# Optimization experiments

Hardware: AMD Instinct MI355X
Metric: run time of the kernel (lower is better)

## Reference

```python
import jax, jax.numpy as jnp
import numpy as np

TAU_PAIR = 1.5
TAU_ATTN = 1.5
TAU_SS = 1.25
TOPK = 3
WIN = 8
EPS = 1e-8
NEG = -10000.0


def _linear(x, w, b):
    return x @ w.T + b


def _mlp2(x, w1, b1, w2, b2):
    return _linear(jax.nn.gelu(_linear(x, w1, b1), approximate=False), w2, b2)


def _layernorm(x, g, b, eps=1e-5):
    m = jnp.mean(x, axis=-1, keepdims=True)
    v = jnp.var(x, axis=-1, keepdims=True)
    return (x - m) / jnp.sqrt(v + eps) * g + b


def _win_mean(vals, mask, radius):
    # vals, mask: (B, L); masked windowed mean via conv1d with ones kernel
    K = 2 * radius + 1
    kern = jnp.ones((1, 1, K), vals.dtype)
    conv = lambda a: jax.lax.conv_general_dilated(
        a, kern, (1,), [(radius, radius)], dimension_numbers=('NCH', 'OIH', 'NCH'))
    sx = conv((vals * mask)[:, None, :])
    sm = conv(mask[:, None, :])
    return (sx / jnp.maximum(sm, 1.0))[:, 0]


def setup_inputs() -> dict:
    key = jax.random.key(0)
    ks = jax.random.split(key, 32)
    B, L, D = 4, 2048, 512
    R = 32
    PLU = R * (R - 1) // 2        # 496
    CURV = 16
    CH1 = max(CURV * 2, PLU // 2)  # 248
    CONT_IN = 3 * D + CURV        # 1552
    CONTENT, STATS_D, BOT = 64, 32, 64
    STATS_IN = 10 + 3 + 8         # N_STATS_V2 + ss_prob + ss_logit_proj

    def w(k, shape):
        return jax.random.normal(k, shape, jnp.float32) * 0.05

    return {
        'H_geom': jax.random.normal(ks[0], (B, L, D), jnp.float32),
        'pair_logits': jax.random.normal(ks[1], (B, L, L), jnp.float32),
        'ss_logits': jax.random.normal(ks[2], (B, L, 3), jnp.float32),
        'kappa_last': jax.random.normal(ks[3], (B, L, PLU), jnp.float32),
        'seq_mask': jnp.ones((B, L), dtype=bool),
        'curv_w1': w(ks[4], (CH1, PLU)), 'curv_b1': jnp.zeros((CH1,), jnp.float32),
        'curv_w2': w(ks[5], (CURV, CH1)), 'curv_b2': jnp.zeros((CURV,), jnp.float32),
        'sslp_w': w(ks[6], (8, 3)), 'sslp_b': jnp.zeros((8,), jnp.float32),
        'ln_g': jnp.ones((10,), jnp.float32), 'ln_b': jnp.zeros((10,), jnp.float32),
        'cont_w1': w(ks[7], (CONTENT * 2, CONT_IN)), 'cont_b1': jnp.zeros((CONTENT * 2,), jnp.float32),
        'cont_w2': w(ks[8], (CONTENT, CONTENT * 2)), 'cont_b2': jnp.zeros((CONTENT,), jnp.float32),
        'stats_w1': w(ks[9], (STATS_D * 2, STATS_IN)), 'stats_b1': jnp.zeros((STATS_D * 2,), jnp.float32),
        'stats_w2': w(ks[10], (STATS_D, STATS_D * 2)), 'stats_b2': jnp.zeros((STATS_D,), jnp.float32),
        'merge_w1': w(ks[11], (BOT * 2, CONTENT + STATS_D)), 'merge_b1': jnp.zeros((BOT * 2,), jnp.float32),
        'merge_w2': w(ks[12], (BOT, BOT * 2)), 'merge_b2': jnp.zeros((BOT,), jnp.float32),
    }


def _forward(H_geom, pair_logits, ss_logits, kappa_last, seq_mask,
             curv_w1, curv_b1, curv_w2, curv_b2, sslp_w, sslp_b, ln_g, ln_b,
             cont_w1, cont_b1, cont_w2, cont_b2, stats_w1, stats_b1, stats_w2, stats_b2,
             merge_w1, merge_b1, merge_w2, merge_b2):
    mf = seq_mask.astype(jnp.float32)  # (B, L)
    B, L, D = H_geom.shape
    smb = seq_mask.astype(bool)
    diag = jnp.eye(L, dtype=bool)[None]
    invalid = diag | (~smb)[:, None, :] | (~smb)[:, :, None]  # (B, L, L)
    clean = jnp.where(invalid, NEG, pair_logits)

    curv = _mlp2(kappa_last, curv_w1, curv_b1, curv_w2, curv_b2)  # (B, L, 16)

    pair_prob = jax.nn.sigmoid(clean / TAU_PAIR)
    pair_attn = jnp.nan_to_num(jax.nn.softmax(clean / TAU_ATTN, axis=-1), nan=0.0)
    pair_entropy = -(pair_attn * jnp.log(pair_attn + EPS)).sum(-1, keepdims=True)
    max_pair_prob = pair_prob.max(-1, keepdims=True)
    unpaired = 1.0 - max_pair_prob
    valid_pair = (~invalid).astype(jnp.float32)
    n_valid = jnp.maximum(valid_pair.sum(-1, keepdims=True), 1.0)
    pair_mass = pair_prob.sum(-1, keepdims=True) / n_valid

    ss_prob = jax.nn.softmax(ss_logits / TAU_SS, axis=-1)
    ss_entropy = -(ss_prob * jnp.log(ss_prob + EPS)).sum(-1, keepdims=True)
    log_n = jnp.maximum(jnp.log(n_valid), 1e-4)
    pen = jnp.nan_to_num(jnp.clip(pair_entropy / log_n, 0.0, 1.0), nan=0.0)
    ss_lp = _linear(ss_logits, sslp_w, sslp_b)

    ctx_mean = jnp.einsum('bij,bjd->bid', pair_attn, H_geom)

    k = min(TOPK, L)
    tv, ti = jax.lax.top_k(clean, k)  # (B, L, k)
    tvalid = (tv > -9000.0).astype(jnp.float32)
    tw = jax.nn.softmax(jnp.where(tvalid == 0, NEG, tv) / TAU_ATTN, axis=-1) * tvalid
    tw = tw / jnp.maximum(tw.sum(-1, keepdims=True), EPS)
    tw = jnp.nan_to_num(tw, nan=0.0)
    H_topk = jax.vmap(lambda h, i: h[i])(H_geom, ti)  # (B, L, k, D)
    ctx_topk = (tw[..., None] * H_topk).sum(axis=2)

    idx = jnp.arange(L)
    dist = jnp.abs(idx[:, None] - idx[None, :]).astype(jnp.float32)[None]
    local = (dist <= WIN).astype(jnp.float32)
    distal = (dist > WIN).astype(jnp.float32)
    n_local = jnp.maximum((valid_pair * local).sum(-1, keepdims=True), 1.0)
    n_distal = jnp.maximum((valid_pair * distal).sum(-1, keepdims=True), 1.0)
    local_mass = (pair_prob * local).sum(-1, keepdims=True) / n_local
    distal_mass = (pair_prob * distal).sum(-1, keepdims=True) / n_distal

    win_up3 = _win_mean(unpaired[..., 0], mf, 2)[..., None]
    win_up7 = _win_mean(unpaired[..., 0], mf, 5)[..., None]
    win_ent7 = _win_mean(pen[..., 0], mf, 5)[..., None]

    stats = jnp.concatenate([
        pair_mass, max_pair_prob, unpaired, pen, ss_entropy,
        local_mass, distal_mass, win_up3, win_up7, win_ent7], axis=-1) * mf[..., None]
    stats = jnp.nan_to_num(stats, nan=0.0, posinf=1.0, neginf=0.0)

    content_in = jnp.concatenate([H_geom, ctx_mean, ctx_topk, curv], axis=-1)
    stats_in = jnp.concatenate([_layernorm(stats, ln_g, ln_b), ss_prob, ss_lp], axis=-1)
    ch = _mlp2(content_in, cont_w1, cont_b1, cont_w2, cont_b2)
    sh = _mlp2(stats_in, stats_w1, stats_b1, stats_w2, stats_b2)
    B_tok = _mlp2(jnp.concatenate([ch, sh], axis=-1), merge_w1, merge_b1, merge_w2, merge_b2)
    B_tok = B_tok * mf[..., None]
    return B_tok, stats


def reference(H_geom, pair_logits, ss_logits, kappa_last, seq_mask,
              curv_w1, curv_b1, curv_w2, curv_b2, sslp_w, sslp_b, ln_g, ln_b,
              cont_w1, cont_b1, cont_w2, cont_b2, stats_w1, stats_b1, stats_w2, stats_b2,
              merge_w1, merge_b1, merge_w2, merge_b2):
    return _forward(H_geom, pair_logits, ss_logits, kappa_last, seq_mask,
                    curv_w1, curv_b1, curv_w2, curv_b2, sslp_w, sslp_b, ln_g, ln_b,
                    cont_w1, cont_b1, cont_w2, cont_b2, stats_w1, stats_b1, stats_w2, stats_b2,
                    merge_w1, merge_b1, merge_w2, merge_b2)
```

## Files before the change

kernel.cpp:

```cpp
#include <hip/hip_runtime.h>
#include <hip/hip_bf16.h>

#define BN 4
#define LL 2048
#define DD 512
#define BLROWS 8192
#define CI_LD 1792

typedef __attribute__((ext_vector_type(8))) short s8v;
typedef __attribute__((ext_vector_type(4))) short s4v;
typedef __attribute__((ext_vector_type(4))) float f4v;

#define GF_GELU    1
#define GF_OUTBF16 2
#define GF_SCALE   4
#define GF_BIAS    8

static __device__ __forceinline__ float frcp(float x) { return __builtin_amdgcn_rcpf(x); }

template<int C>
static __device__ __forceinline__ float fdpp0(float x) {
    return __builtin_bit_cast(float, __builtin_amdgcn_update_dpp(
        0, __builtin_bit_cast(int, x), C, 0xf, 0xf, false));
}
static __device__ __forceinline__ float wave_sum(float x) {
    x += fdpp0<0x111>(x);
    x += fdpp0<0x112>(x);
    x += fdpp0<0x114>(x);
    x += fdpp0<0x118>(x);
    x += fdpp0<0x142>(x);
    x += fdpp0<0x143>(x);
    return __builtin_bit_cast(float, __builtin_amdgcn_readlane(__builtin_bit_cast(int, x), 63));
}
template<int C>
static __device__ __forceinline__ void amax_lev(unsigned& bk, int& bj) {
    unsigned ok = (unsigned)__builtin_amdgcn_update_dpp(0, (int)bk, C, 0xf, 0xf, false);
    int      oj = __builtin_amdgcn_update_dpp(0x7fffffff, bj, C, 0xf, 0xf, false);
    bool take = (ok > bk) || (ok == bk && oj < bj);
    bk = take ? ok : bk;
    bj = take ? oj : bj;
}

struct Seg2 {
    const float* src;
    __hip_bfloat16* dst;
    int srows, scols, sld, drows, dld, pcols, doff, blk0;
};
struct ConvArgs2 {
    Seg2 s[9];
    int nseg;
};

__global__ __launch_bounds__(256) void mega1(
    ConvArgs2 a, int nconv,
    const float* __restrict__ pair, const float* __restrict__ H,
    __hip_bfloat16* __restrict__ E, __hip_bfloat16* __restrict__ ci,
    float* __restrict__ invZ, float* __restrict__ pen, float* __restrict__ unp,
    float* __restrict__ sigs, float* __restrict__ sigloc, float* __restrict__ mpp,
    __hip_bfloat16* __restrict__ Ht,
    const float* __restrict__ curv_w2, const float* __restrict__ cont_w1,
    const float* __restrict__ curv_b2, const float* __restrict__ cont_b1,
    __hip_bfloat16* __restrict__ cont_w1b, float* __restrict__ cbias2)
{
    __shared__ float tile[64][36];
    int bid = blockIdx.x;

    if (bid < 2048) {
        int wid = threadIdx.x >> 6, lane = threadIdx.x & 63;
        int g = bid * 4 + wid;
        int i = g & (LL - 1);
        const float* row = pair + (size_t)g * LL;
        int lb = lane << 2;

        float tt[32];
        float ssig = 0.f, sloc = 0.f, T = 0.f, U = 0.f;
        #pragma unroll
        for (int k = 0; k < 8; ++k) {
            float4 v = *(const float4*)(row + k * 256 + lb);
            float cv4[4] = {v.x, v.y, v.z, v.w};
            #pragma unroll
            for (int t = 0; t < 4; ++t) {
                int j = k * 256 + lb + t;
                float cv = cv4[t];
                float e = __expf(cv * 0.66666667f);
                e = (j == i) ? 0.0f : e;
                tt[k * 4 + t] = e;
                T += e;
                U = fmaf(e, cv, U);
                float sg = e * frcp(1.0f + e);
                ssig += sg;
                int dd = j - i;
                sloc += ((unsigned)(dd + 8) <= 16u) ? sg : 0.0f;
            }
        }
        T    = wave_sum(T);
        U    = wave_sum(U);
        ssig = wave_sum(ssig);
        sloc = wave_sum(sloc);

        int f0 = -1, f1 = -1;
        int fidx[3]; float fval[3];
        #pragma unroll
        for (int p = 0; p < 3; ++p) {
            unsigned bk = 0u; int bj = 0x7fffffff;
            #pragma unroll
            for (int k = 0; k < 8; ++k) {
                #pragma unroll
                for (int t = 0; t < 4; ++t) {
                    int j = k * 256 + lb + t;
                    unsigned mk = __float_as_uint(tt[k * 4 + t]);
                    mk = (j != f0 && j != f1) ? mk : 0u;
                    bool take = (mk > bk) || (mk == bk && j < bj);
                    bk = take ? mk : bk;
                    bj = take ? j : bj;
                }
            }
            amax_lev<0x111>(bk, bj);
            amax_lev<0x112>(bk, bj);
            amax_lev<0x114>(bk, bj);
            amax_lev<0x118>(bk, bj);
            amax_lev<0x142>(bk, bj);
            amax_lev<0x143>(bk, bj);
            unsigned kk = (unsigned)__builtin_amdgcn_readlane((int)bk, 63);
            int jj = __builtin_amdgcn_readlane(bj, 63);
            fval[p] = __uint_as_float(kk);
            fidx[p] = jj;
            if (p == 0) f0 = jj;
            if (p == 1) f1 = jj;
        }
        float t0v = fval[0];
        float s = frcp(t0v);

        short* Eg = (short*)E + (size_t)g * LL;
        #pragma unroll
        for (int k = 0; k < 8; ++k) {
            s4v ev;
            #pragma unroll
            for (int t = 0; t < 4; ++t) {
                __hip_bfloat16 hb = __float2bfloat16(tt[k * 4 + t] * s);
                ev[t] = *(short*)&hb;
            }
            *(s4v*)(Eg + k * 256 + lb) = ev;
        }

        float e1 = fval[1] * s;
        float e2 = fval[2] * s;
        float inv = frcp(1.0f + e1 + e2);
        float w0 = inv, w1 = e1 * inv, w2 = e2 * inv;
        int b = g >> 11;
        const float* Hb = H + (size_t)b * LL * DD;
        int dcol = lane << 3;
        const float* r0p = Hb + (size_t)fidx[0] * DD + dcol;
        const float* r1p = Hb + (size_t)fidx[1] * DD + dcol;
        const float* r2p = Hb + (size_t)fidx[2] * DD + dcol;
        float4 a0 = *(const float4*)(r0p), a1 = *(const float4*)(r0p + 4);
        float4 b0 = *(const float4*)(r1p), b1 = *(const float4*)(r1p + 4);
        float4 c0 = *(const float4*)(r2p), c1 = *(const float4*)(r2p + 4);
        s8v ov;
        float o8[8] = {w0*a0.x + w1*b0.x + w2*c0.x, w0*a0.y + w1*b0.y + w2*c0.y,
                       w0*a0.z + w1*b0.z + w2*c0.z, w0*a0.w + w1*b0.w + w2*c0.w,
                       w0*a1.x + w1*b1.x + w2*c1.x, w0*a1.y + w1*b1.y + w2*c1.y,
                       w0*a1.z + w1*b1.z + w2*c1.z, w0*a1.w + w1*b1.w + w2*c1.w};
        #pragma unroll
        for (int t = 0; t < 8; ++t) {
            __hip_bfloat16 hb = __float2bfloat16(o8[t]);
            ov[t] = *(short*)&hb;
        }
        *(s8v*)((short*)ci + (size_t)g * CI_LD + 1024 + dcol) = ov;

        if (lane == 0) {
            float lnt0 = __logf(t0v);
            float z = s * T;
            float iz = 1.0f / z;
            invZ[g] = iz;
            float s1s = s * (0.66666667f * U - lnt0 * T);
            float ent = __logf(T) - lnt0 - s1s * iz;
            float p = ent * (1.0f / 7.6241224f);
            pen[g] = fminf(fmaxf(p, 0.0f), 1.0f);
            float mp = t0v * frcp(1.0f + t0v);
            mpp[g] = mp;
            unp[g] = 1.0f - mp;
            sigs[g] = ssig;
            sigloc[g] = sloc;
        }
        return;
    }
    bid -= 2048;

    if (bid < nconv) {
        int si = 0;
        #pragma unroll
        for (int k = 1; k < 9; ++k)
            if (k < a.nseg && bid >= a.s[k].blk0) si = k;
        const Seg2 sg = a.s[si];
        int eb = (bid - sg.blk0) * 2048 + threadIdx.x * 8;
        if (eb >= sg.drows * sg.pcols) return;
        int r = eb / sg.pcols;
        int c = eb - r * sg.pcols;
        s8v ov;
        if (r < sg.srows && c >= sg.doff && c + 8 <= sg.doff + sg.scols && (sg.sld & 3) == 0) {
            const float* p = sg.src + (size_t)r * sg.sld + (c - sg.doff);
            float4 x = *(const float4*)p, y = *(const float4*)(p + 4);
            float vv[8] = {x.x, x.y, x.z, x.w, y.x, y.y, y.z, y.w};
            #pragma unroll
            for (int t = 0; t < 8; ++t) {
                __hip_bfloat16 h = __float2bfloat16(vv[t]);
                ov[t] = *(short*)&h;
            }
        } else {
            #pragma unroll
            for (int t = 0; t < 8; ++t) {
                int cc = c + t - sg.doff;
                float v = (r < sg.srows && cc >= 0 && cc < sg.scols)
                          ? sg.src[(size_t)r * sg.sld + cc] : 0.0f;
                __hip_bfloat16 h = __float2bfloat16(v);
                ov[t] = *(short*)&h;
            }
        }
        *(s8v*)((short*)sg.dst + (size_t)r * sg.dld + c) = ov;
        return;
    }
    bid -= nconv;

    if (bid < 2048) {
        int b = bid >> 9;
        int j0 = (bid & 31) * 64, d0 = ((bid >> 5) & 15) * 32;
        const float* Hb = H + (size_t)b * LL * DD;
        int t = threadIdx.x;
        #pragma unroll
        for (int it = 0; it < 2; ++it) {
            int lin = it * 256 + t;
            int j = lin >> 3, s = (lin & 7) << 2;
            float4 v = *(const float4*)(Hb + (size_t)(j0 + j) * DD + d0 + s);
            *(float4*)&tile[j][s] = v;
        }
        __syncthreads();
        {
            int j = t >> 2, d = (t & 3) << 3;
            s8v ov;
            #pragma unroll
            for (int q = 0; q < 8; ++q) {
                __hip_bfloat16 h = __float2bfloat16(tile[j][d + q]);
                ov[q] = *(short*)&h;
            }
            *(s8v*)((short*)ci + (size_t)(b * LL + j0 + j) * CI_LD + d0 + d) = ov;
        }
        {
            int d = t >> 3, j = (t & 7) << 3;
            s8v ov;
            #pragma unroll
            for (int q = 0; q < 8; ++q) {
                __hip_bfloat16 h = __float2bfloat16(tile[j + q][d]);
                ov[q] = *(short*)&h;
            }
            *(s8v*)((short*)Ht + (size_t)b * DD * LL + (size_t)(d0 + d) * LL + j0 + j) = ov;
        }
        return;
    }
    bid -= 2048;

    if (bid < 16) {
        int o8 = bid * 256 + threadIdx.x;
        int n = o8 >> 5, k0 = (o8 & 31) * 8;
        s8v ov;
        #pragma unroll
        for (int t = 0; t < 8; ++t) {
            int k = k0 + t;
            float s = 0.f;
            if (k < 248) {
                #pragma unroll
                for (int c = 0; c < 16; ++c)
                    s = fmaf(curv_w2[c * 248 + k], cont_w1[(size_t)n * 1552 + 1536 + c], s);
            }
            __hip_bfloat16 h = __float2bfloat16(s);
            ov[t] = *(short*)&h;
        }
        *(s8v*)((short*)cont_w1b + (size_t)n * CI_LD + 1536 + k0) = ov;
    } else {
        if (threadIdx.x < 128) {
            int n = threadIdx.x;
            float s = cont_b1[n];
            #pragma unroll
            for (int c = 0; c < 16; ++c)
                s = fmaf(curv_b2[c], cont_w1[(size_t)n * 1552 + 1536 + c], s);
            cbias2[n] = s;
        }
    }
}

template<int TBM, int TBN, int BK, int FM, int FN, int WGN, int NT>
static __device__ __forceinline__ void gemm_body(
    short* sbuf,
    const short* __restrict__ A, const short* __restrict__ Bt,
    const float* __restrict__ bias, const float* __restrict__ rowscale,
    void* __restrict__ C, int N, int K, int NP,
    int lda, int ldb, int ldc,
    long sA, long sB, long sC, long sScale, int flags,
    int m0, int n0, int zb)
{
    constexpr int G  = BK / 8;
    constexpr int GL = (G == 4) ? 2 : 3;
    constexpr int SH = (G == 4) ? 1 : 0;
    constexpr int CHUNKS = (TBM + TBN) * G;
    constexpr int ITER = (CHUNKS + NT - 1) / NT;
    constexpr int SBS = (TBM + TBN) * BK;

    int tid = threadIdx.x;
    int wid = tid >> 6, lane = tid & 63;
    int wm = (wid / WGN) * FM * 16, wn = (wid % WGN) * FN * 16;
    int lr = lane & 15, lk = (lane >> 4) * 8;
    const short* Ab = A + (long)zb * sA;
    const short* Bb = Bt + (long)zb * sB;

    auto issue = [&](int kt, int p) {
        int k0 = kt * BK;
        #pragma unroll
        for (int it = 0; it < ITER; ++it) {
            int cc = it * NT + tid;
            if ((CHUNKS % NT) != 0 && cc >= CHUNKS) break;
            short* lb = sbuf + (size_t)p * SBS + (size_t)(it * NT + (tid & ~63)) * 8;
            const short* gp;
            if (cc < TBM * G) {
                int r = cc >> GL, gs = cc & (G - 1);
                int gg = gs ^ ((r >> SH) & (G - 1));
                gp = Ab + (long)(m0 + r) * lda + k0 + gg * 8;
            } else {
                int c2 = cc - TBM * G;
                int r = c2 >> GL, gs = c2 & (G - 1);
                int gg = gs ^ ((r >> SH) & (G - 1));
                gp = Bb + (long)(n0 + r) * ldb + k0 + gg * 8;
            }
            __builtin_amdgcn_global_load_lds(
                (const __attribute__((address_space(1))) void*)gp,
                (__attribute__((address_space(3))) void*)lb, 16, 0, 0);
        }
    };

    f4v acc[FM][FN];
    #pragma unroll
    for (int i = 0; i < FM; i++)
        #pragma unroll
        for (int j = 0; j < FN; j++) acc[i][j] = {0.f, 0.f, 0.f, 0.f};

    issue(0, 0);
    __syncthreads();
    int KT = K / BK;
    for (int kt = 0; kt < KT; ++kt) {
        int p = kt & 1;
        if (kt + 1 < KT) issue(kt + 1, p ^ 1);
        const short* As = sbuf + (size_t)p * SBS;
        const short* Bs = As + TBM * BK;
        s8v af[FM][BK / 32], bf[FN][BK / 32];
        #pragma unroll
        for (int ks = 0; ks < BK / 32; ++ks) {
            int gg = ks * 4 + (lk >> 3);
            #pragma unroll
            for (int s = 0; s < FM; ++s) {
                int r = wm + s * 16 + lr;
                af[s][ks] = *(const s8v*)(As + ((size_t)r * G + (gg ^ ((r >> SH) & (G - 1)))) * 8);
            }
            #pragma unroll
            for (int s = 0; s < FN; ++s) {
                int r = wn + s * 16 + lr;
                bf[s][ks] = *(const s8v*)(Bs + ((size_t)r * G + (gg ^ ((r >> SH) & (G - 1)))) * 8);
            }
        }
        #pragma unroll
        for (int ks = 0; ks < BK / 32; ++ks)
            #pragma unroll
            for (int i = 0; i < FM; i++)
                #pragma unroll
                for (int j = 0; j < FN; j++)
                    acc[i][j] = __builtin_amdgcn_mfma_f32_16x16x32_bf16(af[i][ks], bf[j][ks], acc[i][j], 0, 0, 0);
        __syncthreads();
    }

    int r0 = (lane >> 4) * 4;
    long cb = (long)zb * sC;
    const float* scale = (flags & GF_SCALE) ? rowscale + (long)zb * sScale : nullptr;
    #pragma unroll
    for (int j = 0; j < FN; j++) {
        int col = n0 + wn + j * 16 + lr;
        if (col >= NP) continue;
        float bv = ((flags & GF_BIAS) && col < N) ? bias[col] : 0.0f;
        #pragma unroll
        for (int i = 0; i < FM; i++) {
            #pragma unroll
            for (int r = 0; r < 4; r++) {
                int row = m0 + wm + i * 16 + r0 + r;
                float v = acc[i][j][r] + bv;
                if (flags & GF_GELU) v = 0.5f * v * (1.0f + erff(v * 0.70710678118f));
                if (flags & GF_SCALE) v *= scale[row];
                if (col >= N) v = 0.0f;
                if (flags & GF_OUTBF16)
                    ((__hip_bfloat16*)C)[cb + (long)row * ldc + col] = __float2bfloat16(v);
                else
                    ((float*)C)[cb + (long)row * ldc + col] = v;
            }
        }
    }
}

template<int TBM, int TBN, int BK, int FM, int FN, int WGN, int NT, int WPE>
__global__ __launch_bounds__(NT, WPE) void gemm_k(
    const short* __restrict__ A, const short* __restrict__ Bt,
    const float* __restrict__ bias, const float* __restrict__ rowscale,
    void* __restrict__ C, int N, int K, int NP,
    int lda, int ldb, int ldc,
    long sA, long sB, long sC, long sScale, int flags)
{
    __shared__ __align__(16) short sb[2 * (TBM + TBN) * BK];
    gemm_body<TBM, TBN, BK, FM, FN, WGN, NT>(
        sb, A, Bt, bias, rowscale, C, N, K, NP, lda, ldb, ldc,
        sA, sB, sC, sScale, flags,
        blockIdx.x * TBM, blockIdx.y * TBN, blockIdx.z);
}

__global__ __launch_bounds__(512, 4) void mega2(
    const short* __restrict__ E, const short* __restrict__ Ht,
    const float* __restrict__ invZ, __hip_bfloat16* __restrict__ ci,
    const short* __restrict__ kappa_b, const short* __restrict__ curv_w1b,
    const float* __restrict__ curv_b1,
    const float* __restrict__ ss_logits, const float* __restrict__ sslp_w,
    const float* __restrict__ sslp_b, const float* __restrict__ ln_g,
    const float* __restrict__ ln_b,
    const float* __restrict__ pen, const float* __restrict__ unp,
    const float* __restrict__ sigs, const float* __restrict__ sigloc,
    const float* __restrict__ mpp,
    const float* __restrict__ cont_b2, const float* __restrict__ stats_b2,
    const float* __restrict__ stats_w1, const float* __restrict__ stats_b1,
    float* __restrict__ cbias, float* __restrict__ stats_out,
    __hip_bfloat16* __restrict__ A2)
{
    __shared__ __align__(16) short sb[32768];
    int bid = blockIdx.x;
    int tid = threadIdx.x;

    if (bid < 256) {
        int m0 = (bid & 15) * 128, n0 = ((bid >> 4) & 3) * 128, zb = bid >> 6;
        gemm_body<128, 128, 64, 4, 2, 4, 512>(
            sb, E, Ht, nullptr, invZ, (void*)(ci + 512),
            512, LL, 512, LL, LL, CI_LD,
            (long)LL * LL, (long)DD * LL, (long)LL * CI_LD, (long)LL,
            GF_OUTBF16 | GF_SCALE, m0, n0, zb);
        return;
    }
    if (bid < 512) {
        int id = bid - 256;
        int m0 = (id & 127) * 64, n0 = (id >> 7) * 128;
        gemm_body<64, 128, 64, 2, 2, 4, 512>(
            sb, kappa_b, curv_w1b, curv_b1, nullptr, (void*)(ci + 1536),
            248, 512, 256, 512, 512, CI_LD,
            0, 0, 0, 0, GF_OUTBF16 | GF_GELU | GF_BIAS, m0, n0, 0);
        return;
    }

    int sid = bid - 512;
    float* ws = (float*)sb;
    for (int k = tid; k < 64 * 21 + 64; k += 512)
        ws[k] = (k < 64 * 21) ? stats_w1[k] : stats_b1[k - 64 * 21];
    if (sid == 0 && tid < 128) {
        cbias[tid] = (tid < 64) ? cont_b2[tid] : (tid < 96 ? stats_b2[tid - 64] : 0.0f);
    }
    __syncthreads();

    int g = sid * 512 + tid;
    int i = g & (LL - 1);
    int b = g >> 11;
    const float* unpb = unp + ((size_t)b << 11);
    const float* penb = pen + ((size_t)b << 11);

    auto wmean = [&](const float* a2, int rad) -> float {
        int lo = i - rad; if (lo < 0) lo = 0;
        int hi = i + rad; if (hi > LL - 1) hi = LL - 1;
        float s = 0.f;
        for (int j = lo; j <= hi; ++j) s += a2[j];
        return s / (float)(hi - lo + 1);
    };
    float w3 = wmean(unpb, 2);
    float w7 = wmean(unpb, 5);
    float e7 = wmean(penb, 5);

    float n_valid = 2047.0f;
    float pm = sigs[g] / n_valid;
    int lo8 = i - 8; if (lo8 < 0) lo8 = 0;
    int hi8 = i + 8; if (hi8 > LL - 1) hi8 = LL - 1;
    float nl = (float)(hi8 - lo8);
    float local_mass  = sigloc[g] / fmaxf(nl, 1.0f);
    float distal_mass = (sigs[g] - sigloc[g]) / fmaxf(n_valid - nl, 1.0f);

    float s0 = ss_logits[(size_t)g * 3 + 0];
    float s1 = ss_logits[(size_t)g * 3 + 1];
    float s2 = ss_logits[(size_t)g * 3 + 2];
    float sm = fmaxf(s0, fmaxf(s1, s2));
    float p0 = __expf((s0 - sm) * 0.8f);
    float p1 = __expf((s1 - sm) * 0.8f);
    float p2 = __expf((s2 - sm) * 0.8f);
    float ips = 1.0f / (p0 + p1 + p2);
    p0 *= ips; p1 *= ips; p2 *= ips;
    float ss_ent = -(p0 * __logf(p0 + 1e-8f) + p1 * __logf(p1 + 1e-8f) + p2 * __logf(p2 + 1e-8f));

    float st[10];
    st[0] = pm; st[1] = mpp[g]; st[2] = unp[g]; st[3] = penb[i];
    st[4] = ss_ent; st[5] = local_mass; st[6] = distal_mass;
    st[7] = w3; st[8] = w7; st[9] = e7;

    float* so = stats_out + (size_t)g * 10;
    #pragma unroll
    for (int k = 0; k < 10; ++k) so[k] = st[k];

    float mean = 0.f;
    #pragma unroll
    for (int k = 0; k < 10; ++k) mean += st[k];
    mean *= 0.1f;
    float var = 0.f;
    #pragma unroll
    for (int k = 0; k < 10; ++k) { float d = st[k] - mean; var += d * d; }
    var *= 0.1f;
    float rstd = 1.0f / sqrtf(var + 1e-5f);

    float x[21];
    #pragma unroll
    for (int k = 0; k < 10; ++k)
        x[k] = (st[k] - mean) * rstd * ln_g[k] + ln_b[k];
    x[10] = p0; x[11] = p1; x[12] = p2;
    #pragma unroll
    for (int o = 0; o < 8; ++o)
        x[13 + o] = sslp_b[o] + sslp_w[o * 3] * s0 + sslp_w[o * 3 + 1] * s1 + sslp_w[o * 3 + 2] * s2;

    short* arow = (short*)A2 + (size_t)g * 192 + 128;
    #pragma unroll
    for (int o8 = 0; o8 < 8; ++o8) {
        s8v ov;
        #pragma unroll
        for (int oo = 0; oo < 8; ++oo) {
            int o = o8 * 8 + oo;
            float s = ws[64 * 21 + o];
            #pragma unroll
            for (int k = 0; k < 21; ++k) s = fmaf(ws[o * 21 + k], x[k], s);
            s = 0.5f * s * (1.0f + erff(s * 0.70710678118f));
            __hip_bfloat16 h = __float2bfloat16(s);
            ov[oo] = *(short*)&h;
        }
        *(s8v*)(arow + o8 * 8) = ov;
    }
}

__global__ __launch_bounds__(256) void tail_kernel(
    const short* __restrict__ A2,
    const short* __restrict__ B2,
    const float* __restrict__ cbias,
    const short* __restrict__ mw1,
    const float* __restrict__ mb1,
    const short* __restrict__ mw2,
    const float* __restrict__ mb2,
    float* __restrict__ out)
{
    __shared__ __align__(16) short md[16][136];
    __shared__ __align__(16) short am[16][136];
    int tid = threadIdx.x;
    int w = tid >> 6, lane = tid & 63;
    int lr = lane & 15;
    int lk = (lane >> 4) * 8;
    int r0 = (lane >> 4) * 4;
    long rb = (long)blockIdx.x * 16;

    f4v a1[2] = {{0.f,0.f,0.f,0.f},{0.f,0.f,0.f,0.f}};
    {
        const short* ap  = A2 + (size_t)(rb + lr) * 192 + lk;
        const short* bp0 = B2 + (size_t)(w * 32 + lr) * 192 + lk;
        const short* bp1 = bp0 + 16 * 192;
        #pragma unroll
        for (int ks = 0; ks < 6; ++ks) {
            s8v a  = *(const s8v*)(ap  + ks * 32);
            s8v b0 = *(const s8v*)(bp0 + ks * 32);
            s8v b1 = *(const s8v*)(bp1 + ks * 32);
            a1[0] = __builtin_amdgcn_mfma_f32_16x16x32_bf16(a, b0, a1[0], 0, 0, 0);
            a1[1] = __builtin_amdgcn_mfma_f32_16x16x32_bf16(a, b1, a1[1], 0, 0, 0);
        }
    }
    #pragma unroll
    for (int j = 0; j < 2; ++j) {
        int col = w * 32 + j * 16 + lr;
        float bv = cbias[col];
        #pragma unroll
        for (int r = 0; r < 4; ++r) {
            __hip_bfloat16 h = __float2bfloat16(a1[j][r] + bv);
            md[r0 + r][col] = *(short*)&h;
        }
    }
    __syncthreads();

    f4v a2[2] = {{0.f,0.f,0.f,0.f},{0.f,0.f,0.f,0.f}};
    {
        const short* cp0 = mw1 + (size_t)(w * 32 + lr) * 128 + lk;
        const short* cp1 = cp0 + 16 * 128;
        #pragma unroll
        for (int ks = 0; ks < 4; ++ks) {
            s8v a  = *(const s8v*)(&md[lr][ks * 32 + lk]);
            s8v b0 = *(const s8v*)(cp0 + ks * 32);
            s8v b1 = *(const s8v*)(cp1 + ks * 32);
            a2[0] = __builtin_amdgcn_mfma_f32_16x16x32_bf16(a, b0, a2[0], 0, 0, 0);
            a2[1] = __builtin_amdgcn_mfma_f32_16x16x32_bf16(a, b1, a2[1], 0, 0, 0);
        }
    }
    #pragma unroll
    for (int j = 0; j < 2; ++j) {
        int col = w * 32 + j * 16 + lr;
        float bv = mb1[col];
        #pragma unroll
        for (int r = 0; r < 4; ++r) {
            float v = a2[j][r] + bv;
            v = 0.5f * v * (1.0f + erff(v * 0.70710678118f));
            __hip_bfloat16 h = __float2bfloat16(v);
            am[r0 + r][col] = *(short*)&h;
        }
    }
    __syncthreads();

    f4v a3 = {0.f, 0.f, 0.f, 0.f};
    {
        const short* dp = mw2 + (size_t)(w * 16 + lr) * 128 + lk;
        #pragma unroll
        for (int ks = 0; ks < 4; ++ks) {
            s8v a = *(const s8v*)(&am[lr][ks * 32 + lk]);
            s8v b = *(const s8v*)(dp + ks * 32);
            a3 = __builtin_amdgcn_mfma_f32_16x16x32_bf16(a, b, a3, 0, 0, 0);
        }
    }
    int col = w * 16 + lr;
    float bv = mb2[col];
    #pragma unroll
    for (int r = 0; r < 4; ++r)
        out[(rb + r0 + r) * 64 + col] = a3[r] + bv;
}

extern "C" void kernel_launch(void* const* d_in, const int* in_sizes, int n_in,
                              void* d_out, int out_size, void* d_ws, size_t ws_size,
                              hipStream_t stream) {
    const float* H         = (const float*)d_in[0];
    const float* pair      = (const float*)d_in[1];
    const float* ss_logits = (const float*)d_in[2];
    const float* kappa     = (const float*)d_in[3];
    const float* curv_w1   = (const float*)d_in[5];
    const float* curv_b1   = (const float*)d_in[6];
    const float* curv_w2   = (const float*)d_in[7];
    const float* curv_b2   = (const float*)d_in[8];
    const float* sslp_w    = (const float*)d_in[9];
    const float* sslp_b    = (const float*)d_in[10];
    const float* ln_g      = (const float*)d_in[11];
    const float* ln_b      = (const float*)d_in[12];
    const float* cont_w1   = (const float*)d_in[13];
    const float* cont_b1   = (const float*)d_in[14];
    const float* cont_w2   = (const float*)d_in[15];
    const float* cont_b2   = (const float*)d_in[16];
    const float* stats_w1  = (const float*)d_in[17];
    const float* stats_b1  = (const float*)d_in[18];
    const float* stats_w2  = (const float*)d_in[19];
    const float* stats_b2  = (const float*)d_in[20];
    const float* merge_w1  = (const float*)d_in[21];
    const float* merge_b1  = (const float*)d_in[22];
    const float* merge_w2  = (const float*)d_in[23];
    const float* merge_b2  = (const float*)d_in[24];

    char* w = (char*)d_ws;
    size_t off = 0;
    auto alloc = [&](size_t n) -> void* {
        void* p = w + off;
        off = (off + n + 255) & ~(size_t)255;
        return p;
    };

    __hip_bfloat16* E         = (__hip_bfloat16*)alloc((size_t)BN * LL * LL * 2);
    __hip_bfloat16* Ht        = (__hip_bfloat16*)alloc((size_t)BN * DD * LL * 2);
    __hip_bfloat16* ci        = (__hip_bfloat16*)alloc((size_t)BLROWS * CI_LD * 2);
    __hip_bfloat16* kappa_b   = (__hip_bfloat16*)alloc((size_t)BLROWS * 512 * 2);
    __hip_bfloat16* A2        = (__hip_bfloat16*)alloc((size_t)BLROWS * 192 * 2);
    __hip_bfloat16* curv_w1b  = (__hip_bfloat16*)alloc(256 * 512 * 2);
    __hip_bfloat16* cont_w1b  = (__hip_bfloat16*)alloc(128 * CI_LD * 2);
    __hip_bfloat16* B2        = (__hip_bfloat16*)alloc(128 * 192 * 2);
    __hip_bfloat16* merge_w1b = (__hip_bfloat16*)alloc(128 * 128 * 2);
    __hip_bfloat16* merge_w2b = (__hip_bfloat16*)alloc(64 * 128 * 2);
    float* cbias    = (float*)alloc(128 * 4);
    float* cbias2   = (float*)alloc(128 * 4);
    float* r_invZ   = (float*)alloc(BLROWS * 4);
    float* r_pen    = (float*)alloc(BLROWS * 4);
    float* r_unp    = (float*)alloc(BLROWS * 4);
    float* r_sig    = (float*)alloc(BLROWS * 4);
    float* r_sigloc = (float*)alloc(BLROWS * 4);
    float* r_mpp    = (float*)alloc(BLROWS * 4);

    ConvArgs2 ca;
    auto mkseg = [](const float* s, __hip_bfloat16* d, int srows, int scols,
                    int sld, int drows, int dld, int pcols, int doff) -> Seg2 {
        Seg2 g; g.src = s; g.dst = d; g.srows = srows; g.scols = scols;
        g.sld = sld; g.drows = drows; g.dld = dld; g.pcols = pcols;
        g.doff = doff; g.blk0 = 0;
        return g;
    };
    ca.s[0] = mkseg(curv_w1,  curv_w1b,  248, 496, 496,  256, 512, 512, 0);
    ca.s[1] = mkseg(cont_w1,  cont_w1b,  128, 1536, 1552, 128, CI_LD, 1536, 0);
    ca.s[2] = mkseg(cont_w2,  B2,        64,  128, 128,  64,  192, 192, 0);
    ca.s[3] = mkseg(stats_w2, B2 + 64 * 192, 32, 64, 64, 64, 192, 192, 128);
    ca.s[4] = mkseg(merge_w1, merge_w1b, 128, 96,  96,   128, 128, 128, 0);
    ca.s[5] = mkseg(merge_w2, merge_w2b, 64,  128, 128,  64,  128, 128, 0);
    ca.s[6] = mkseg(kappa,    kappa_b,   BLROWS, 496, 496, BLROWS, 512, 512, 0);
    ca.nseg = 7;
    int nconv = 0;
    for (int s = 0; s < 7; ++s) {
        ca.s[s].blk0 = nconv;
        nconv += (ca.s[s].drows * ca.s[s].pcols + 2047) / 2048;
    }

    mega1<<<2048 + nconv + 2048 + 17, 256, 0, stream>>>(
        ca, nconv, pair, H, E, ci,
        r_invZ, r_pen, r_unp, r_sig, r_sigloc, r_mpp, Ht,
        curv_w2, cont_w1, curv_b2, cont_b1, cont_w1b, cbias2);

    mega2<<<528, 512, 0, stream>>>(
        (const short*)E, (const short*)Ht, r_invZ, ci,
        (const short*)kappa_b, (const short*)curv_w1b, curv_b1,
        ss_logits, sslp_w, sslp_b, ln_g, ln_b,
        r_pen, r_unp, r_sig, r_sigloc, r_mpp,
        cont_b2, stats_b2, stats_w1, stats_b1,
        cbias, (float*)d_out + (size_t)BLROWS * 64, A2);

    auto* g_content = gemm_k<32, 128, 64, 2, 2, 4, 256, 4>;
    g_content<<<dim3(BLROWS / 32, 1, 1), 256, 0, stream>>>(
        (const short*)ci, (const short*)cont_w1b, cbias2, nullptr, A2,
        128, CI_LD, 128, CI_LD, CI_LD, 192, 0, 0, 0, 0,
        GF_OUTBF16 | GF_GELU | GF_BIAS);

    tail_kernel<<<BLROWS / 16, 256, 0, stream>>>(
        (const short*)A2, (const short*)B2, cbias,
        (const short*)merge_w1b, merge_b1,
        (const short*)merge_w2b, merge_b2,
        (float*)d_out);
}
```

Before: 257.6 us.

## Fuse content GEMM into tail kernel, single-pass top-3, interleave row blocks

The content MLP first-layer GEMM and the merge tail now run in one kernel. The GEMM epilogue writes into shared memory, so the A2 intermediate no longer makes a global round trip and one launch is removed. In mega1, top-3 selection is tracked per lane during the exp pass, replacing three extra scans over 32 registers. E is also stored unnormalized, which removes the later rescale pass, and the entropy formula is simplified to match. Row-processing blocks are interleaved with conversion blocks to balance the work. The cost is a change in E's scale, which downstream code must now absorb via invZ, and higher LDS use per block in the fused kernel.

```diff
diff --git a/kernel.cpp b/kernel.cpp
--- a/kernel.cpp
+++ b/kernel.cpp
@@ -15,6 +15,7 @@
 #define GF_OUTBF16 2
 #define GF_SCALE   4
 #define GF_BIAS    8
+#define GF_OUTLDS  16
 
 static __device__ __forceinline__ float frcp(float x) { return __builtin_amdgcn_rcpf(x); }
 
@@ -63,58 +64,62 @@
     __hip_bfloat16* __restrict__ cont_w1b, float* __restrict__ cbias2)
 {
     __shared__ float tile[64][36];
-    int bid = blockIdx.x;
-
-    if (bid < 2048) {
+    int raw = blockIdx.x;
+    bool isrow;
+    int bid;
+    if (raw < 4096) { isrow = !(raw & 1); bid = raw >> 1; }
+    else            { isrow = false;      bid = raw - 2048; }
+
+    if (isrow) {
         int wid = threadIdx.x >> 6, lane = threadIdx.x & 63;
         int g = bid * 4 + wid;
         int i = g & (LL - 1);
         const float* row = pair + (size_t)g * LL;
         int lb = lane << 2;
-
-        float tt[32];
+        short* Eg = (short*)E + (size_t)g * LL;
+
         float ssig = 0.f, sloc = 0.f, T = 0.f, U = 0.f;
+        unsigned q0 = 0u, q1 = 0u, q2 = 0u;
+        int u0 = 0x7fffffff, u1 = 0x7fffffff, u2 = 0x7fffffff;
         #pragma unroll
         for (int k = 0; k < 8; ++k) {
             float4 v = *(const float4*)(row + k * 256 + lb);
             float cv4[4] = {v.x, v.y, v.z, v.w};
+            s4v ev;
             #pragma unroll
             for (int t = 0; t < 4; ++t) {
                 int j = k * 256 + lb + t;
                 float cv = cv4[t];
                 float e = __expf(cv * 0.66666667f);
                 e = (j == i) ? 0.0f : e;
-                tt[k * 4 + t] = e;
+                __hip_bfloat16 hb = __float2bfloat16(e);
+                ev[t] = *(short*)&hb;
                 T += e;
                 U = fmaf(e, cv, U);
                 float sg = e * frcp(1.0f + e);
                 ssig += sg;
                 int dd = j - i;
                 sloc += ((unsigned)(dd + 8) <= 16u) ? sg : 0.0f;
-            }
+                unsigned mk = __float_as_uint(e);
+                bool c0 = mk > q0, c1 = mk > q1, c2 = mk > q2;
+                q2 = c1 ? q1 : (c2 ? mk : q2);  u2 = c1 ? u1 : (c2 ? j : u2);
+                q1 = c0 ? q0 : (c1 ? mk : q1);  u1 = c0 ? u0 : (c1 ? j : u1);
+                q0 = c0 ? mk : q0;              u0 = c0 ? j  : u0;
+            }
+            *(s4v*)(Eg + k * 256 + lb) = ev;
         }
         T    = wave_sum(T);
         U    = wave_sum(U);
         ssig = wave_sum(ssig);
         sloc = wave_sum(sloc);
 
-        int f0 = -1, f1 = -1;
         int fidx[3]; float fval[3];
+        int cnt = 0;
         #pragma unroll
         for (int p = 0; p < 3; ++p) {
-            unsigned bk = 0u; int bj = 0x7fffffff;
-            #pragma unroll
-            for (int k = 0; k < 8; ++k) {
-                #pragma unroll
-                for (int t = 0; t < 4; ++t) {
-                    int j = k * 256 + lb + t;
-                    unsigned mk = __float_as_uint(tt[k * 4 + t]);
-                    mk = (j != f0 && j != f1) ? mk : 0u;
-                    bool take = (mk > bk) || (mk == bk && j < bj);
-                    bk = take ? mk : bk;
-                    bj = take ? j : bj;
-                }
-            }
+            unsigned ck = (cnt == 0) ? q0 : (cnt == 1 ? q1 : (cnt == 2 ? q2 : 0u));
+            int      cj = (cnt == 0) ? u0 : (cnt == 1 ? u1 : (cnt == 2 ? u2 : 0x7fffffff));
+            unsigned bk = ck; int bj = cj;
             amax_lev<0x111>(bk, bj);
             amax_lev<0x112>(bk, bj);
             amax_lev<0x114>(bk, bj);
@@ -125,23 +130,10 @@
             int jj = __builtin_amdgcn_readlane(bj, 63);
             fval[p] = __uint_as_float(kk);
             fidx[p] = jj;
-            if (p == 0) f0 = jj;
-            if (p == 1) f1 = jj;
+            cnt += (cj == jj) ? 1 : 0;
         }
         float t0v = fval[0];
         float s = frcp(t0v);
-
-        short* Eg = (short*)E + (size_t)g * LL;
-        #pragma unroll
-        for (int k = 0; k < 8; ++k) {
-            s4v ev;
-            #pragma unroll
-            for (int t = 0; t < 4; ++t) {
-                __hip_bfloat16 hb = __float2bfloat16(tt[k * 4 + t] * s);
-                ev[t] = *(short*)&hb;
-            }
-            *(s4v*)(Eg + k * 256 + lb) = ev;
-        }
 
         float e1 = fval[1] * s;
         float e2 = fval[2] * s;
@@ -169,12 +161,9 @@
         *(s8v*)((short*)ci + (size_t)g * CI_LD + 1024 + dcol) = ov;
 
         if (lane == 0) {
-            float lnt0 = __logf(t0v);
-            float z = s * T;
-            float iz = 1.0f / z;
+            float iz = 1.0f / T;
             invZ[g] = iz;
-            float s1s = s * (0.66666667f * U - lnt0 * T);
-            float ent = __logf(T) - lnt0 - s1s * iz;
+            float ent = __logf(T) - 0.66666667f * U * iz;
             float p = ent * (1.0f / 7.6241224f);
             pen[g] = fminf(fmaxf(p, 0.0f), 1.0f);
             float mp = t0v * frcp(1.0f + t0v);
@@ -185,7 +174,6 @@
         }
         return;
     }
-    bid -= 2048;
 
     if (bid < nconv) {
         int si = 0;
@@ -296,7 +284,8 @@
     void* __restrict__ C, int N, int K, int NP,
     int lda, int ldb, int ldc,
     long sA, long sB, long sC, long sScale, int flags,
-    int m0, int n0, int zb)
+    int m0, int n0, int zb,
+    short* ldsC = nullptr, int ldsLd = 0)
 {
     constexpr int G  = BK / 8;
     constexpr int GL = (G == 4) ? 2 : 3;
@@ -390,6 +379,11 @@
                 int row = m0 + wm + i * 16 + r0 + r;
                 float v = acc[i][j][r] + bv;
                 if (flags & GF_GELU) v = 0.5f * v * (1.0f + erff(v * 0.70710678118f));
+                if (flags & GF_OUTLDS) {
+                    __hip_bfloat16 h = __float2bfloat16(v);
+                    ldsC[(size_t)(wm + i * 16 + r0 + r) * ldsLd + col] = *(short*)&h;
+                    continue;
+                }
                 if (flags & GF_SCALE) v *= scale[row];
                 if (col >= N) v = 0.0f;
                 if (flags & GF_OUTBF16)
@@ -399,21 +393,6 @@
             }
         }
     }
-}
-
-template<int TBM, int TBN, int BK, int FM, int FN, int WGN, int NT, int WPE>
-__global__ __launch_bounds__(NT, WPE) void gemm_k(
-    const short* __restrict__ A, const short* __restrict__ Bt,
-    const float* __restrict__ bias, const float* __restrict__ rowscale,
-    void* __restrict__ C, int N, int K, int NP,
-    int lda, int ldb, int ldc,
-    long sA, long sB, long sC, long sScale, int flags)
-{
-    __shared__ __align__(16) short sb[2 * (TBM + TBN) * BK];
-    gemm_body<TBM, TBN, BK, FM, FN, WGN, NT>(
-        sb, A, Bt, bias, rowscale, C, N, K, NP, lda, ldb, ldc,
-        sA, sB, sC, sScale, flags,
-        blockIdx.x * TBM, blockIdx.y * TBN, blockIdx.z);
 }
 
 __global__ __launch_bounds__(512, 4) void mega2(
@@ -430,7 +409,7 @@
     const float* __restrict__ cont_b2, const float* __restrict__ stats_b2,
     const float* __restrict__ stats_w1, const float* __restrict__ stats_b1,
     float* __restrict__ cbias, float* __restrict__ stats_out,
-    __hip_bfloat16* __restrict__ A2)
+    __hip_bfloat16* __restrict__ SHo)
 {
     __shared__ __align__(16) short sb[32768];
     int bid = blockIdx.x;
@@ -528,7 +507,7 @@
     for (int o = 0; o < 8; ++o)
         x[13 + o] = sslp_b[o] + sslp_w[o * 3] * s0 + sslp_w[o * 3 + 1] * s1 + sslp_w[o * 3 + 2] * s2;
 
-    short* arow = (short*)A2 + (size_t)g * 192 + 128;
+    short* arow = (short*)SHo + (size_t)g * 64;
     #pragma unroll
     for (int o8 = 0; o8 < 8; ++o8) {
         s8v ov;
@@ -546,37 +525,49 @@
     }
 }
 
-__global__ __launch_bounds__(256) void tail_kernel(
-    const short* __restrict__ A2,
-    const short* __restrict__ B2,
-    const float* __restrict__ cbias,
-    const short* __restrict__ mw1,
-    const float* __restrict__ mb1,
-    const short* __restrict__ mw2,
-    const float* __restrict__ mb2,
+__global__ __launch_bounds__(256, 2) void fused_ct(
+    const short* __restrict__ ci, const short* __restrict__ cont_w1b,
+    const float* __restrict__ cbias2,
+    const short* __restrict__ SHi,
+    const short* __restrict__ B2, const float* __restrict__ cbias,
+    const short* __restrict__ mw1, const float* __restrict__ mb1,
+    const short* __restrict__ mw2, const float* __restrict__ mb2,
     float* __restrict__ out)
 {
-    __shared__ __align__(16) short md[16][136];
-    __shared__ __align__(16) short am[16][136];
+    __shared__ __align__(16) short sb[20480];
+    __shared__ __align__(16) short A2t[32 * 196];
+    short* md = sb;
+    short* am = sb + 32 * 136;
+
     int tid = threadIdx.x;
     int w = tid >> 6, lane = tid & 63;
-    int lr = lane & 15;
-    int lk = (lane >> 4) * 8;
-    int r0 = (lane >> 4) * 4;
-    long rb = (long)blockIdx.x * 16;
-
-    f4v a1[2] = {{0.f,0.f,0.f,0.f},{0.f,0.f,0.f,0.f}};
+    int lr = lane & 15, lk = (lane >> 4) * 8, r0 = (lane >> 4) * 4;
+    long rb = (long)blockIdx.x * 32;
+
     {
-        const short* ap  = A2 + (size_t)(rb + lr) * 192 + lk;
-        const short* bp0 = B2 + (size_t)(w * 32 + lr) * 192 + lk;
-        const short* bp1 = bp0 + 16 * 192;
-        #pragma unroll
-        for (int ks = 0; ks < 6; ++ks) {
-            s8v a  = *(const s8v*)(ap  + ks * 32);
-            s8v b0 = *(const s8v*)(bp0 + ks * 32);
-            s8v b1 = *(const s8v*)(bp1 + ks * 32);
-            a1[0] = __builtin_amdgcn_mfma_f32_16x16x32_bf16(a, b0, a1[0], 0, 0, 0);
-            a1[1] = __builtin_amdgcn_mfma_f32_16x16x32_bf16(a, b1, a1[1], 0, 0, 0);
+        int r = tid >> 3, c = (tid & 7) << 3;
+        s8v v = *(const s8v*)(SHi + (size_t)(rb + r) * 64 + c);
+        *(s8v*)(A2t + r * 196 + 128 + c) = v;
+    }
+
+    gemm_body<32, 128, 64, 2, 2, 4, 256>(
+        sb, ci, cont_w1b, cbias2, nullptr, nullptr,
+        128, 1792, 128, CI_LD, CI_LD, 0,
+        0, 0, 0, 0, GF_GELU | GF_BIAS | GF_OUTLDS,
+        (int)rb, 0, 0, A2t, 196);
+    __syncthreads();
+
+    f4v c1[2][2] = {{{0.f,0.f,0.f,0.f},{0.f,0.f,0.f,0.f}},
+                    {{0.f,0.f,0.f,0.f},{0.f,0.f,0.f,0.f}}};
+    #pragma unroll
+    for (int ks = 0; ks < 6; ++ks) {
+        s8v b0 = *(const s8v*)(B2 + (size_t)(w * 32 + lr) * 192 + ks * 32 + lk);
+        s8v b1 = *(const s8v*)(B2 + (size_t)(w * 32 + 16 + lr) * 192 + ks * 32 + lk);
+        #pragma unroll
+        for (int i2 = 0; i2 < 2; ++i2) {
+            s8v a = *(const s8v*)(A2t + (i2 * 16 + lr) * 196 + ks * 32 + lk);
+            c1[i2][0] = __builtin_amdgcn_mfma_f32_16x16x32_bf16(a, b0, c1[i2][0], 0, 0, 0);
+            c1[i2][1] = __builtin_amdgcn_mfma_f32_16x16x32_bf16(a, b1, c1[i2][1], 0, 0, 0);
         }
     }
     #pragma unroll
@@ -584,55 +575,62 @@
         int col = w * 32 + j * 16 + lr;
         float bv = cbias[col];
         #pragma unroll
-        for (int r = 0; r < 4; ++r) {
-            __hip_bfloat16 h = __float2bfloat16(a1[j][r] + bv);
-            md[r0 + r][col] = *(short*)&h;
-        }
+        for (int i2 = 0; i2 < 2; ++i2)
+            #pragma unroll
+            for (int r = 0; r < 4; ++r) {
+                __hip_bfloat16 h = __float2bfloat16(c1[i2][j][r] + bv);
+                md[(i2 * 16 + r0 + r) * 136 + col] = *(short*)&h;
+            }
     }
     __syncthreads();
 
-    f4v a2[2] = {{0.f,0.f,0.f,0.f},{0.f,0.f,0.f,0.f}};
-    {
-        const short* cp0 = mw1 + (size_t)(w * 32 + lr) * 128 + lk;
-        const short* cp1 = cp0 + 16 * 128;
-        #pragma unroll
-        for (int ks = 0; ks < 4; ++ks) {
-            s8v a  = *(const s8v*)(&md[lr][ks * 32 + lk]);
-            s8v b0 = *(const s8v*)(cp0 + ks * 32);
-            s8v b1 = *(const s8v*)(cp1 + ks * 32);
-            a2[0] = __builtin_amdgcn_mfma_f32_16x16x32_bf16(a, b0, a2[0], 0, 0, 0);
-            a2[1] = __builtin_amdgcn_mfma_f32_16x16x32_bf16(a, b1, a2[1], 0, 0, 0);
-        }
-    }
+    f4v c2a[2][2] = {{{0.f,0.f,0.f,0.f},{0.f,0.f,0.f,0.f}},
+                     {{0.f,0.f,0.f,0.f},{0.f,0.f,0.f,0.f}}};
+    #pragma unroll
+    for (int ks = 0; ks < 4; ++ks) {
+        s8v b0 = *(const s8v*)(mw1 + (size_t)(w * 32 + lr) * 128 + ks * 32 + lk);
+        s8v b1 = *(const s8v*)(mw1 + (size_t)(w * 32 + 16 + lr) * 128 + ks * 32 + lk);
+        #pragma unroll
+        for (int i2 = 0; i2 < 2; ++i2) {
+            s8v a = *(const s8v*)(md + (i2 * 16 + lr) * 136 + ks * 32 + lk);
+            c2a[i2][0] = __builtin_amdgcn_mfma_f32_16x16x32_bf16(a, b0, c2a[i2][0], 0, 0, 0);
+            c2a[i2][1] = __builtin_amdgcn_mfma_f32_16x16x32_bf16(a, b1, c2a[i2][1], 0, 0, 0);
+        }
+    }
+    __syncthreads();
     #pragma unroll
     for (int j = 0; j < 2; ++j) {
         int col = w * 32 + j * 16 + lr;
         float bv = mb1[col];
         #pragma unroll
-        for (int r = 0; r < 4; ++r) {
-            float v = a2[j][r] + bv;
-            v = 0.5f * v * (1.0f + erff(v * 0.70710678118f));
-            __hip_bfloat16 h = __float2bfloat16(v);
-            am[r0 + r][col] = *(short*)&h;
-        }
+        for (int i2 = 0; i2 < 2; ++i2)
+            #pragma unroll
+            for (int r = 0; r < 4; ++r) {
+                float v = c2a[i2][j][r] + bv;
+                v = 0.5f * v * (1.0f + erff(v * 0.70710678118f));
+                __hip_bfloat16 h = __float2bfloat16(v);
+                am[(i2 * 16 + r0 + r) * 136 + col] = *(short*)&h;
+            }
     }
     __syncthreads();
 
-    f4v a3 = {0.f, 0.f, 0.f, 0.f};
-    {
-        const short* dp = mw2 + (size_t)(w * 16 + lr) * 128 + lk;
-        #pragma unroll
-        for (int ks = 0; ks < 4; ++ks) {
-            s8v a = *(const s8v*)(&am[lr][ks * 32 + lk]);
-            s8v b = *(const s8v*)(dp + ks * 32);
-            a3 = __builtin_amdgcn_mfma_f32_16x16x32_bf16(a, b, a3, 0, 0, 0);
+    f4v c3[2] = {{0.f,0.f,0.f,0.f},{0.f,0.f,0.f,0.f}};
+    #pragma unroll
+    for (int ks = 0; ks < 4; ++ks) {
+        s8v b = *(const s8v*)(mw2 + (size_t)(w * 16 + lr) * 128 + ks * 32 + lk);
+        #pragma unroll
+        for (int i2 = 0; i2 < 2; ++i2) {
+            s8v a = *(const s8v*)(am + (i2 * 16 + lr) * 136 + ks * 32 + lk);
+            c3[i2] = __builtin_amdgcn_mfma_f32_16x16x32_bf16(a, b, c3[i2], 0, 0, 0);
         }
     }
     int col = w * 16 + lr;
     float bv = mb2[col];
     #pragma unroll
-    for (int r = 0; r < 4; ++r)
-        out[(rb + r0 + r) * 64 + col] = a3[r] + bv;
+    for (int i2 = 0; i2 < 2; ++i2)
+        #pragma unroll
+        for (int r = 0; r < 4; ++r)
+            out[(rb + i2 * 16 + r0 + r) * 64 + col] = c3[i2][r] + bv;
 }
 
 extern "C" void kernel_launch(void* const* d_in, const int* in_sizes, int n_in,
@@ -675,7 +673,7 @@
     __hip_bfloat16* Ht        = (__hip_bfloat16*)alloc((size_t)BN * DD * LL * 2);
     __hip_bfloat16* ci        = (__hip_bfloat16*)alloc((size_t)BLROWS * CI_LD * 2);
     __hip_bfloat16* kappa_b   = (__hip_bfloat16*)alloc((size_t)BLROWS * 512 * 2);
-    __hip_bfloat16* A2        = (__hip_bfloat16*)alloc((size_t)BLROWS * 192 * 2);
+    __hip_bfloat16* SH        = (__hip_bfloat16*)alloc((size_t)BLROWS * 64 * 2);
     __hip_bfloat16* curv_w1b  = (__hip_bfloat16*)alloc(256 * 512 * 2);
     __hip_bfloat16* cont_w1b  = (__hip_bfloat16*)alloc(128 * CI_LD * 2);
     __hip_bfloat16* B2        = (__hip_bfloat16*)alloc(128 * 192 * 2);
@@ -723,16 +721,11 @@
         ss_logits, sslp_w, sslp_b, ln_g, ln_b,
         r_pen, r_unp, r_sig, r_sigloc, r_mpp,
         cont_b2, stats_b2, stats_w1, stats_b1,
-        cbias, (float*)d_out + (size_t)BLROWS * 64, A2);
-
-    auto* g_content = gemm_k<32, 128, 64, 2, 2, 4, 256, 4>;
-    g_content<<<dim3(BLROWS / 32, 1, 1), 256, 0, stream>>>(
-        (const short*)ci, (const short*)cont_w1b, cbias2, nullptr, A2,
-        128, CI_LD, 128, CI_LD, CI_LD, 192, 0, 0, 0, 0,
-        GF_OUTBF16 | GF_GELU | GF_BIAS);
-
-    tail_kernel<<<BLROWS / 16, 256, 0, stream>>>(
-        (const short*)A2, (const short*)B2, cbias,
+        cbias, (float*)d_out + (size_t)BLROWS * 64, SH);
+
+    fused_ct<<<BLROWS / 32, 256, 0, stream>>>(
+        (const short*)ci, (const short*)cont_w1b, cbias2,
+        (const short*)SH, (const short*)B2, cbias,
         (const short*)merge_w1b, merge_b1,
         (const short*)merge_w2b, merge_b2,
         (float*)d_out);
```

Result: slower. 265.4 us (+3.0%).
